# Optimization experiments

Measured on AMD Instinct MI355X. Metric: run time of the kernel, lower is better.

## Reference

```python
import jax, jax.numpy as jnp
import numpy as np

B, S, D, H = 2, 4096, 1024, 16
DH = D // H            # head dim = 64
W = 256                # one-sided attention window (attention_window // 2)
NC = S // W            # number of query chunks
NEG = -1e9


def setup_inputs() -> dict:
    key = jax.random.key(0)
    ks = jax.random.split(key, 8)
    sc = 0.02
    return {
        "hidden_states": jax.random.normal(ks[0], (B, S, D), jnp.float32),
        # additive float mask: 0 = local token, <0 = padding, >0 = global. All zeros here.
        "attention_mask": jnp.zeros((B, 1, 1, S), jnp.float32),
        "Wq": jax.random.normal(ks[1], (D, D), jnp.float32) * sc,
        "bq": jnp.zeros((D,), jnp.float32),
        "Wk": jax.random.normal(ks[2], (D, D), jnp.float32) * sc,
        "bk": jnp.zeros((D,), jnp.float32),
        "Wv": jax.random.normal(ks[3], (D, D), jnp.float32) * sc,
        "bv": jnp.zeros((D,), jnp.float32),
        "Wo": jax.random.normal(ks[4], (D, D), jnp.float32) * sc,
        "bo": jnp.zeros((D,), jnp.float32),
    }


def _heads(x, w, b):
    # [B,S,D] -> [B,H,S,DH]
    return (x @ w + b).reshape(B, S, H, DH).transpose(0, 2, 1, 3)


def _forward(hidden_states, attention_mask, Wq, bq, Wk, bk, Wv, bv, Wo, bo):
    mask = attention_mask[:, 0, 0, :]                    # [B,S] additive key mask
    q = _heads(hidden_states, Wq, bq) / jnp.sqrt(jnp.float32(DH))
    k = _heads(hidden_states, Wk, bk)
    v = _heads(hidden_states, Wv, bv)

    # Overlapping key/value chunks: chunk c covers padded positions [c*W, c*W+3W),
    # i.e. global keys [c*W - W, c*W + 2W) -- the union of the windows of its W queries.
    idx = jnp.arange(NC)[:, None] * W + jnp.arange(3 * W)[None, :]   # [NC,3W] into padded axis
    k_pad = jnp.pad(k, ((0, 0), (0, 0), (W, W), (0, 0)))
    v_pad = jnp.pad(v, ((0, 0), (0, 0), (W, W), (0, 0)))
    k_ch = k_pad[:, :, idx]                               # [B,H,NC,3W,DH]
    v_ch = v_pad[:, :, idx]                               # [B,H,NC,3W,DH]
    mask_ch = jnp.pad(mask, ((0, 0), (W, W)))[:, idx]     # [B,NC,3W]

    q_ch = q.reshape(B, H, NC, W, DH)
    scores = jnp.einsum('bhcqd,bhckd->bhcqk', q_ch, k_ch)  # [B,H,NC,W,3W]

    # Band mask: query local p attends key local o with 0 <= o - p <= 2W.
    rel = jnp.arange(3 * W)[None, :] - jnp.arange(W)[:, None]        # [W,3W]
    band = (rel >= 0) & (rel <= 2 * W)
    key_gidx = idx - W                                               # global key index
    valid = (key_gidx >= 0) & (key_gidx < S)                         # [NC,3W]
    allowed = band[None, :, :] & valid[:, None, :]                   # [NC,W,3W]

    scores = scores + mask_ch[:, None, :, None, :]
    scores = jnp.where(allowed[None, None], scores, NEG)
    probs = jax.nn.softmax(scores, axis=-1)

    out = jnp.einsum('bhcqk,bhckd->bhcqd', probs, v_ch)    # [B,H,NC,W,DH]
    out = out.reshape(B, H, S, DH).transpose(0, 2, 1, 3).reshape(B, S, D)
    return out @ Wo + bo


def reference(hidden_states, attention_mask, Wq, bq, Wk, bk, Wv, bv, Wo, bo):
    return _forward(hidden_states, attention_mask, Wq, bq, Wk, bk, Wv, bv, Wo, bo)
```

## Files before the change

### kernel.cpp

```cpp
#include <hip/hip_runtime.h>

typedef unsigned short u16;
typedef __bf16 bf16x8 __attribute__((ext_vector_type(8)));
typedef u16 u16x8 __attribute__((ext_vector_type(8)));
typedef float f32x4 __attribute__((ext_vector_type(4)));
typedef unsigned uint2v __attribute__((ext_vector_type(2)));

#define LOG2E 1.4426950408889634f

static __device__ __forceinline__ u16 f2bf(float f) {
    union { float f; unsigned u; } x; x.f = f;
    unsigned r = x.u + 0x7fffu + ((x.u >> 16) & 1u);
    return (u16)(r >> 16);
}

static __device__ __forceinline__ unsigned cvtpk(float lo, float hi) {
    unsigned r;
    asm("v_cvt_pk_bf16_f32 %0, %1, %2" : "=v"(r) : "v"(lo), "v"(hi));
    return r;
}

static __device__ __forceinline__ void gl_lds16(const void* g, void* l) {
    __builtin_amdgcn_global_load_lds(
        (const __attribute__((address_space(1))) void*)g,
        (__attribute__((address_space(3))) void*)l, 16, 0, 0);
}

__global__ __launch_bounds__(256) void cvt_k(const float* __restrict__ src,
                                             u16* __restrict__ dst, int n) {
    int i = (blockIdx.x * 256 + threadIdx.x) * 4;
    if (i < n) {
        float4 v = *(const float4*)(src + i);
        ushort4 o;
        o.x = f2bf(v.x); o.y = f2bf(v.y); o.z = f2bf(v.z); o.w = f2bf(v.w);
        *(ushort4*)(dst + i) = o;
    }
}

__global__ __launch_bounds__(256) void transw_k(const float* __restrict__ w0,
                                                const float* __restrict__ w1,
                                                const float* __restrict__ w2,
                                                const float* __restrict__ w3,
                                                u16* __restrict__ wt) {
    __shared__ float T[64][65];
    const float* src = (blockIdx.z == 0) ? w0 : (blockIdx.z == 1) ? w1
                     : (blockIdx.z == 2) ? w2 : w3;
    u16* dst = wt + (size_t)blockIdx.z * 1048576;
    const int k0 = blockIdx.x * 64, n0 = blockIdx.y * 64;
    const int rr = threadIdx.x >> 6, col = threadIdx.x & 63;
#pragma unroll
    for (int i = 0; i < 16; ++i) {
        int row = i * 4 + rr;
        T[row][col] = src[(size_t)(k0 + row) * 1024 + n0 + col];
    }
    __syncthreads();
#pragma unroll
    for (int i = 0; i < 16; ++i) {
        int row = i * 4 + rr;
        dst[(size_t)(n0 + row) * 1024 + k0 + col] = f2bf(T[col][row]);
    }
}

template<int MODE>
__global__ __launch_bounds__(256) void gemm_t(
    const u16* __restrict__ A, const u16* __restrict__ WT0,
    const float* __restrict__ b0, const float* __restrict__ b1,
    u16* __restrict__ o0, u16* __restrict__ o1, float* __restrict__ oF) {
    __shared__ alignas(16) u16 Al[128 * 64];
    __shared__ alignas(16) u16 Bl[128 * 64];

    const int tid = threadIdx.x;
    const int lane = tid & 63;
    const int wv = tid >> 6;
    const int wr = wv >> 1, wc = wv & 1;
    const int l15 = lane & 15, l4 = lane >> 4;

    const int mbase = blockIdx.x * 128;
    const int sel = (MODE == 0) ? (blockIdx.y >> 3) : 0;
    const int nb = (blockIdx.y & 7) * 128;

    const u16* Ab = A + (size_t)mbase * 1024;
    const u16* Bb = WT0 + (size_t)sel * 1048576 + (size_t)nb * 1024;

    const int lr8 = lane >> 3;
    const int ls = lane & 7;

    f32x4 acc[4][4] = {};

    auto stage = [&](const u16* src, u16* dstL, int k0) {
#pragma unroll
        for (int i = 0; i < 4; ++i) {
            int r = i * 32 + wv * 8 + lr8;
            gl_lds16(src + (size_t)r * 1024 + k0 + ((ls ^ (r & 7)) * 8),
                     dstL + (i * 2048 + wv * 512));
        }
    };

    for (int k0 = 0; k0 < 1024; k0 += 64) {
        stage(Ab, Al, k0);
        stage(Bb, Bl, k0);
        __syncthreads();

#pragma unroll
        for (int ks = 0; ks < 2; ++ks) {
            bf16x8 af[4], bfr[4];
#pragma unroll
            for (int mr = 0; mr < 4; ++mr) {
                int r = wr * 64 + mr * 16 + l15;
                af[mr] = *(const bf16x8*)(Al + r * 64 + (((ks * 4 + l4) ^ (r & 7)) * 8));
            }
#pragma unroll
            for (int nr = 0; nr < 4; ++nr) {
                int r = wc * 64 + nr * 16 + l15;
                bfr[nr] = *(const bf16x8*)(Bl + r * 64 + (((ks * 4 + l4) ^ (r & 7)) * 8));
            }
            if constexpr (MODE == 2) {
#pragma unroll
                for (int mr = 0; mr < 4; ++mr)
#pragma unroll
                    for (int nr = 0; nr < 4; ++nr)
                        acc[mr][nr] = __builtin_amdgcn_mfma_f32_16x16x32_bf16(
                            bfr[nr], af[mr], acc[mr][nr], 0, 0, 0);
            } else {
#pragma unroll
                for (int mr = 0; mr < 4; ++mr)
#pragma unroll
                    for (int nr = 0; nr < 4; ++nr)
                        acc[mr][nr] = __builtin_amdgcn_mfma_f32_16x16x32_bf16(
                            af[mr], bfr[nr], acc[mr][nr], 0, 0, 0);
            }
        }
        __syncthreads();
    }

    if constexpr (MODE == 2) {
#pragma unroll
        for (int mr = 0; mr < 4; ++mr) {
            int srow2 = mbase + wr * 64 + mr * 16 + l15;
            int b_ = srow2 >> 12, s_ = srow2 & 4095;
#pragma unroll
            for (int nr = 0; nr < 4; ++nr) {
                f32x4 bvv = *(const f32x4*)(b0 + nb + wc * 64 + nr * 16 + l4 * 4);
#pragma unroll
                for (int j = 0; j < 4; ++j) {
                    int c2 = nb + wc * 64 + nr * 16 + l4 * 4 + j;
                    float v = acc[mr][nr][j] + bvv[j];
                    o0[(((size_t)(b_ * 16 + (c2 >> 6)) * 64 + (c2 & 63)) * 4096) + s_] = f2bf(v);
                }
            }
        }
        return;
    }

    const float* bias = (MODE == 0 && sel == 1) ? b1 : b0;
    u16* oH = (sel == 0) ? o0 : o1;
    const float scale = (MODE == 0 && sel == 0) ? 0.125f * LOG2E : 1.0f;

#pragma unroll
    for (int mr = 0; mr < 4; ++mr)
#pragma unroll
        for (int nr = 0; nr < 4; ++nr) {
            int col = nb + wc * 64 + nr * 16 + l15;
            float bv_ = bias[col];
#pragma unroll
            for (int j = 0; j < 4; ++j) {
                int row = mbase + wr * 64 + mr * 16 + l4 * 4 + j;
                float v = (acc[mr][nr][j] + bv_) * scale;
                if constexpr (MODE == 0) {
                    int b_ = row >> 12, s_ = row & 4095;
                    int h_ = col >> 6, d_ = col & 63;
                    oH[(((size_t)(b_ * 16 + h_) * 4096) + s_) * 64 + d_] = f2bf(v);
                } else {
                    oF[(size_t)row * 1024 + col] = v;
                }
            }
        }
}

__global__ __launch_bounds__(256) void attn_k(
    const u16* __restrict__ Qh, const u16* __restrict__ Kh,
    const u16* __restrict__ Vt, const float* __restrict__ mask,
    u16* __restrict__ attnb) {
    __shared__ alignas(16) u16 Kt[2][4096];
    __shared__ alignas(16) u16 VtL[2][4096];
    __shared__ alignas(16) u16 Pl[4][2][1024];
    __shared__ alignas(16) float maskl[640];

    const int tid = threadIdx.x;
    const int lane = tid & 63;
    const int wv = tid >> 6;
    const int hw = blockIdx.x;
    const int lg = (hw & 7) * 128 + (hw >> 3);
    const int c = lg & 31;
    const int h = (lg >> 5) & 15;
    const int b = lg >> 9;

    const size_t bh = (size_t)(b * 16 + h) * 4096;
    const u16* Qb = Qh + bh * 64;
    const u16* Kb = Kh + bh * 64;
    const u16* Vb = Vt + bh * 64;
    const float* mb = mask + b * 4096;

    const int l15 = lane & 15;
    const int l4 = lane >> 4;
    const int qbase = c * 128 + wv * 32;
    const int gkbase = c * 128 - 256;

    bf16x8 qf[2][2];
#pragma unroll
    for (int qt = 0; qt < 2; ++qt)
#pragma unroll
        for (int kc = 0; kc < 2; ++kc)
            qf[qt][kc] = *(const bf16x8*)(Qb + (size_t)(qbase + qt * 16 + l15) * 64 + kc * 32 + l4 * 8);

    f32x4 Ov[4][2] = {};
    float lsum[2] = {0.f, 0.f};
    float m[2] = {-3.0e38f, -3.0e38f};

    auto stageK = [&](int buf, int gk) {
#pragma unroll
        for (int i = 0; i < 2; ++i) {
            int r = i * 32 + wv * 8 + (lane >> 3);
            int s = lane & 7;
            int key = min(max(gk + r, 0), 4095);
            gl_lds16(Kb + (size_t)key * 64 + ((s ^ (r & 7)) * 8),
                     &Kt[buf][(i * 32 + wv * 8) * 64]);
        }
    };
    auto stageV = [&](int buf, int gk) {
#pragma unroll
        for (int i = 0; i < 2; ++i) {
            int d = i * 32 + wv * 8 + (lane >> 3);
            int s = lane & 7;
            int col = min(max(gk + ((s ^ (d & 7)) * 8), 0), 4088);
            gl_lds16(Vb + (size_t)d * 4096 + col, &VtL[buf][(i * 32 + wv * 8) * 64]);
        }
    };

    stageK(0, gkbase);
    stageV(0, gkbase);
    for (int i = tid; i < 640; i += 256) {
        int gm = gkbase + i;
        maskl[i] = (gm >= 0 && gm < 4096) ? mb[gm] * LOG2E : 0.f;
    }
    __syncthreads();

    const int tmin = wv >> 1;
    const int tmaxw = 8 + (wv >> 1);

    for (int t = 0; t < 10; ++t) {
        const int cur = t & 1, nxt = cur ^ 1;
        const int gk0 = gkbase + t * 64;
        if (t < 9) { stageK(nxt, gk0 + 64); stageV(nxt, gk0 + 64); }

        if (t >= tmin && t <= tmaxw) {
            f32x4 mv[4];
#pragma unroll
            for (int kb = 0; kb < 4; ++kb)
                mv[kb] = *(const f32x4*)(maskl + t * 64 + kb * 16 + l4 * 4);

            f32x4 sc[4][2] = {};
            __builtin_amdgcn_s_setprio(1);
#pragma unroll
            for (int kc = 0; kc < 2; ++kc)
#pragma unroll
                for (int kb = 0; kb < 4; ++kb) {
                    int r = kb * 16 + l15;
                    bf16x8 kf = *(const bf16x8*)(&Kt[cur][r * 64 + (((kc * 4 + l4) ^ (r & 7)) * 8)]);
                    sc[kb][0] = __builtin_amdgcn_mfma_f32_16x16x32_bf16(kf, qf[0][kc], sc[kb][0], 0, 0, 0);
                    sc[kb][1] = __builtin_amdgcn_mfma_f32_16x16x32_bf16(kf, qf[1][kc], sc[kb][1], 0, 0, 0);
                }
            __builtin_amdgcn_s_setprio(0);

            const int dkq = gk0 - qbase;
            const bool full = (dkq >= -225) && (dkq <= 193) && (gk0 >= 0) && (gk0 <= 4032);
            if (full) {
#pragma unroll
                for (int kb = 0; kb < 4; ++kb)
#pragma unroll
                    for (int qt = 0; qt < 2; ++qt)
#pragma unroll
                        for (int j = 0; j < 4; ++j)
                            sc[kb][qt][j] += mv[kb][j];
            } else {
                const int kb0 = gk0 + l4 * 4;
                const int ub0 = kb0 - (qbase + l15) + 256;
#pragma unroll
                for (int kb = 0; kb < 4; ++kb)
#pragma unroll
                    for (int qt = 0; qt < 2; ++qt)
#pragma unroll
                        for (int j = 0; j < 4; ++j) {
                            float sv = sc[kb][qt][j] + mv[kb][j];
                            unsigned band = (unsigned)(ub0 + kb * 16 + j - qt * 16);
                            unsigned keyv = (unsigned)(kb0 + kb * 16 + j);
                            bool ok = (band <= 512u) && (keyv < 4096u);
                            sc[kb][qt][j] = ok ? sv : -3.0e9f;
                        }
            }

#pragma unroll
            for (int qt = 0; qt < 2; ++qt) {
                u16* Pw = &Pl[wv][qt][0];
                const int prow = l15 * 64;
                float mx = sc[0][qt][0];
#pragma unroll
                for (int kb = 0; kb < 4; ++kb)
#pragma unroll
                    for (int j = 0; j < 4; ++j) mx = fmaxf(mx, sc[kb][qt][j]);
                if (!__all(mx <= m[qt] + 8.0f)) {
                    mx = fmaxf(mx, __shfl_xor(mx, 16));
                    mx = fmaxf(mx, __shfl_xor(mx, 32));
                    float mnew = fmaxf(m[qt], mx);
                    float alpha = exp2f(m[qt] - mnew);
                    m[qt] = mnew;
                    lsum[qt] *= alpha;
#pragma unroll
                    for (int nd = 0; nd < 4; ++nd) Ov[nd][qt] *= alpha;
                }

                float s0 = 0.f;
#pragma unroll
                for (int kb = 0; kb < 4; ++kb) {
                    float p0 = exp2f(sc[kb][qt][0] - m[qt]);
                    float p1 = exp2f(sc[kb][qt][1] - m[qt]);
                    float p2 = exp2f(sc[kb][qt][2] - m[qt]);
                    float p3 = exp2f(sc[kb][qt][3] - m[qt]);
                    s0 += (p0 + p1) + (p2 + p3);
                    uint2v pk;
                    pk[0] = cvtpk(p0, p1);
                    pk[1] = cvtpk(p2, p3);
                    int g = (((kb * 2 + (l4 >> 1)) ^ (l15 & 7)) * 8) + (l4 & 1) * 4;
                    *(uint2v*)(Pw + prow + g) = pk;
                }
                lsum[qt] += s0;
            }

#pragma unroll
            for (int kc = 0; kc < 2; ++kc) {
                bf16x8 vf[4];
#pragma unroll
                for (int nd = 0; nd < 4; ++nd) {
                    int r2 = nd * 16 + l15;
                    vf[nd] = *(const bf16x8*)(&VtL[cur][r2 * 64 +
                        (((kc * 4 + l4) ^ (r2 & 7)) * 8)]);
                }
#pragma unroll
                for (int qt = 0; qt < 2; ++qt) {
                    bf16x8 pf = *(const bf16x8*)(&Pl[wv][qt][0] + l15 * 64 +
                                                 (((kc * 4 + l4) ^ (l15 & 7)) * 8));
                    __builtin_amdgcn_s_setprio(1);
#pragma unroll
                    for (int nd = 0; nd < 4; ++nd)
                        Ov[nd][qt] = __builtin_amdgcn_mfma_f32_16x16x32_bf16(vf[nd], pf, Ov[nd][qt], 0, 0, 0);
                    __builtin_amdgcn_s_setprio(0);
                }
            }
        }
        __syncthreads();
    }

    lsum[0] += __shfl_xor(lsum[0], 16);
    lsum[0] += __shfl_xor(lsum[0], 32);
    lsum[1] += __shfl_xor(lsum[1], 16);
    lsum[1] += __shfl_xor(lsum[1], 32);
    float inv0 = 1.0f / lsum[0];
    float inv1 = 1.0f / lsum[1];
#pragma unroll
    for (int qt = 0; qt < 2; ++qt) {
        float inv = qt ? inv1 : inv0;
        size_t rowb = ((size_t)b * 4096 + qbase + qt * 16 + l15) * 1024 + h * 64 + l4 * 4;
#pragma unroll
        for (int nd = 0; nd < 4; ++nd) {
            uint2v o;
            o[0] = cvtpk(Ov[nd][qt][0] * inv, Ov[nd][qt][1] * inv);
            o[1] = cvtpk(Ov[nd][qt][2] * inv, Ov[nd][qt][3] * inv);
            *(uint2v*)(&attnb[rowb + nd * 16]) = o;
        }
    }
}

extern "C" void kernel_launch(void* const* d_in, const int* in_sizes, int n_in,
                              void* d_out, int out_size, void* d_ws, size_t ws_size,
                              hipStream_t stream) {
    (void)in_sizes; (void)n_in; (void)out_size; (void)ws_size;
    const float* hid  = (const float*)d_in[0];
    const float* mask = (const float*)d_in[1];
    const float* Wq = (const float*)d_in[2];
    const float* bq = (const float*)d_in[3];
    const float* Wk = (const float*)d_in[4];
    const float* bk = (const float*)d_in[5];
    const float* Wv = (const float*)d_in[6];
    const float* bv = (const float*)d_in[7];
    const float* Wo = (const float*)d_in[8];
    const float* bo = (const float*)d_in[9];
    float* out = (float*)d_out;

    char* ws = (char*)d_ws;
    u16* hidb  = (u16*)(ws);
    u16* wt    = (u16*)(ws + (16u << 20));
    u16* Qh    = (u16*)(ws + (24u << 20));
    u16* Kh    = (u16*)(ws + (40u << 20));
    u16* Vtb   = (u16*)(ws + (56u << 20));
    u16* attnb = (u16*)(ws + (72u << 20));

    cvt_k<<<dim3(8192), dim3(256), 0, stream>>>(hid, hidb, 8388608);
    transw_k<<<dim3(16, 16, 4), dim3(256), 0, stream>>>(Wq, Wk, Wv, Wo, wt);
    gemm_t<0><<<dim3(64, 16), dim3(256), 0, stream>>>(hidb, wt, bq, bk,
                                                      Qh, Kh, (float*)nullptr);
    gemm_t<2><<<dim3(64, 8), dim3(256), 0, stream>>>(hidb, wt + 2 * 1048576, bv, (const float*)nullptr,
                                                     Vtb, (u16*)nullptr, (float*)nullptr);
    attn_k<<<dim3(1024), dim3(256), 0, stream>>>(Qh, Kh, Vtb, mask, attnb);
    gemm_t<1><<<dim3(64, 8), dim3(256), 0, stream>>>(attnb, wt + 3 * 1048576, bo, (const float*)nullptr,
                                                     (u16*)nullptr, (u16*)nullptr, out);
}
```

Before: 163.9 us.

## Fuse V projection into QK GEMM launch and skip zero-mask additions in attention

The separate V-projection GEMM launch is folded into the Q/K projection launch by extending the grid to 24 column blocks. Blocks with sel==2 run the swapped-operand MFMA loop and write the transposed V layout. This removes one kernel launch and its tail, and gives a larger grid. The attention kernel now checks whether any mask value in the block's window is nonzero and skips loading and adding the mask when all are zero, at the cost of one extra barrier and a shared flag.

```diff
diff --git a/kernel.cpp b/kernel.cpp
--- a/kernel.cpp
+++ b/kernel.cpp
@@ -7,6 +7,8 @@
 typedef unsigned uint2v __attribute__((ext_vector_type(2)));
 
 #define LOG2E 1.4426950408889634f
+
+template<bool B> struct BoolC { static constexpr bool value = B; };
 
 static __device__ __forceinline__ u16 f2bf(float f) {
     union { float f; unsigned u; } x; x.f = f;
@@ -65,7 +67,9 @@
 __global__ __launch_bounds__(256) void gemm_t(
     const u16* __restrict__ A, const u16* __restrict__ WT0,
     const float* __restrict__ b0, const float* __restrict__ b1,
-    u16* __restrict__ o0, u16* __restrict__ o1, float* __restrict__ oF) {
+    const float* __restrict__ b2,
+    u16* __restrict__ o0, u16* __restrict__ o1, u16* __restrict__ o2,
+    float* __restrict__ oF) {
     __shared__ alignas(16) u16 Al[128 * 64];
     __shared__ alignas(16) u16 Bl[128 * 64];
 
@@ -96,61 +100,66 @@
         }
     };
 
-    for (int k0 = 0; k0 < 1024; k0 += 64) {
-        stage(Ab, Al, k0);
-        stage(Bb, Bl, k0);
-        __syncthreads();
-
-#pragma unroll
-        for (int ks = 0; ks < 2; ++ks) {
-            bf16x8 af[4], bfr[4];
-#pragma unroll
-            for (int mr = 0; mr < 4; ++mr) {
-                int r = wr * 64 + mr * 16 + l15;
-                af[mr] = *(const bf16x8*)(Al + r * 64 + (((ks * 4 + l4) ^ (r & 7)) * 8));
-            }
-#pragma unroll
-            for (int nr = 0; nr < 4; ++nr) {
-                int r = wc * 64 + nr * 16 + l15;
-                bfr[nr] = *(const bf16x8*)(Bl + r * 64 + (((ks * 4 + l4) ^ (r & 7)) * 8));
-            }
-            if constexpr (MODE == 2) {
-#pragma unroll
-                for (int mr = 0; mr < 4; ++mr)
-#pragma unroll
-                    for (int nr = 0; nr < 4; ++nr)
-                        acc[mr][nr] = __builtin_amdgcn_mfma_f32_16x16x32_bf16(
-                            bfr[nr], af[mr], acc[mr][nr], 0, 0, 0);
-            } else {
-#pragma unroll
-                for (int mr = 0; mr < 4; ++mr)
-#pragma unroll
-                    for (int nr = 0; nr < 4; ++nr)
-                        acc[mr][nr] = __builtin_amdgcn_mfma_f32_16x16x32_bf16(
-                            af[mr], bfr[nr], acc[mr][nr], 0, 0, 0);
-            }
-        }
-        __syncthreads();
-    }
-
-    if constexpr (MODE == 2) {
+    auto kloop = [&](auto swap_c) {
+        constexpr bool SWAP = decltype(swap_c)::value;
+        for (int k0 = 0; k0 < 1024; k0 += 64) {
+            stage(Ab, Al, k0);
+            stage(Bb, Bl, k0);
+            __syncthreads();
+#pragma unroll
+            for (int ks = 0; ks < 2; ++ks) {
+                bf16x8 af[4], bfr[4];
+#pragma unroll
+                for (int mr = 0; mr < 4; ++mr) {
+                    int r = wr * 64 + mr * 16 + l15;
+                    af[mr] = *(const bf16x8*)(Al + r * 64 + (((ks * 4 + l4) ^ (r & 7)) * 8));
+                }
+#pragma unroll
+                for (int nr = 0; nr < 4; ++nr) {
+                    int r = wc * 64 + nr * 16 + l15;
+                    bfr[nr] = *(const bf16x8*)(Bl + r * 64 + (((ks * 4 + l4) ^ (r & 7)) * 8));
+                }
+                if constexpr (SWAP) {
+#pragma unroll
+                    for (int mr = 0; mr < 4; ++mr)
+#pragma unroll
+                        for (int nr = 0; nr < 4; ++nr)
+                            acc[mr][nr] = __builtin_amdgcn_mfma_f32_16x16x32_bf16(
+                                bfr[nr], af[mr], acc[mr][nr], 0, 0, 0);
+                } else {
+#pragma unroll
+                    for (int mr = 0; mr < 4; ++mr)
+#pragma unroll
+                        for (int nr = 0; nr < 4; ++nr)
+                            acc[mr][nr] = __builtin_amdgcn_mfma_f32_16x16x32_bf16(
+                                af[mr], bfr[nr], acc[mr][nr], 0, 0, 0);
+                }
+            }
+            __syncthreads();
+        }
+    };
+
+    if (MODE == 0 && sel == 2) {
+        kloop(BoolC<true>{});
 #pragma unroll
         for (int mr = 0; mr < 4; ++mr) {
             int srow2 = mbase + wr * 64 + mr * 16 + l15;
             int b_ = srow2 >> 12, s_ = srow2 & 4095;
 #pragma unroll
             for (int nr = 0; nr < 4; ++nr) {
-                f32x4 bvv = *(const f32x4*)(b0 + nb + wc * 64 + nr * 16 + l4 * 4);
+                f32x4 bvv = *(const f32x4*)(b2 + nb + wc * 64 + nr * 16 + l4 * 4);
 #pragma unroll
                 for (int j = 0; j < 4; ++j) {
                     int c2 = nb + wc * 64 + nr * 16 + l4 * 4 + j;
                     float v = acc[mr][nr][j] + bvv[j];
-                    o0[(((size_t)(b_ * 16 + (c2 >> 6)) * 64 + (c2 & 63)) * 4096) + s_] = f2bf(v);
+                    o2[(((size_t)(b_ * 16 + (c2 >> 6)) * 64 + (c2 & 63)) * 4096) + s_] = f2bf(v);
                 }
             }
         }
         return;
     }
+
+    kloop(BoolC<false>{});
 
     const float* bias = (MODE == 0 && sel == 1) ? b1 : b0;
     u16* oH = (sel == 0) ? o0 : o1;
@@ -185,6 +194,7 @@
     __shared__ alignas(16) u16 VtL[2][4096];
     __shared__ alignas(16) u16 Pl[4][2][1024];
     __shared__ alignas(16) float maskl[640];
+    __shared__ int anymask;
 
     const int tid = threadIdx.x;
     const int lane = tid & 63;
@@ -237,13 +247,23 @@
         }
     };
 
+    if (tid == 0) anymask = 0;
+    __syncthreads();
+
     stageK(0, gkbase);
     stageV(0, gkbase);
-    for (int i = tid; i < 640; i += 256) {
-        int gm = gkbase + i;
-        maskl[i] = (gm >= 0 && gm < 4096) ? mb[gm] * LOG2E : 0.f;
+    {
+        int f = 0;
+        for (int i = tid; i < 640; i += 256) {
+            int gm = gkbase + i;
+            float v = (gm >= 0 && gm < 4096) ? mb[gm] : 0.f;
+            f |= (v != 0.f);
+            maskl[i] = v * LOG2E;
+        }
+        if (f) anymask = 1;
     }
     __syncthreads();
+    const bool useMask = (anymask != 0);
 
     const int tmin = wv >> 1;
     const int tmaxw = 8 + (wv >> 1);
@@ -254,11 +274,6 @@
         if (t < 9) { stageK(nxt, gk0 + 64); stageV(nxt, gk0 + 64); }
 
         if (t >= tmin && t <= tmaxw) {
-            f32x4 mv[4];
-#pragma unroll
-            for (int kb = 0; kb < 4; ++kb)
-                mv[kb] = *(const f32x4*)(maskl + t * 64 + kb * 16 + l4 * 4);
-
             f32x4 sc[4][2] = {};
             __builtin_amdgcn_s_setprio(1);
 #pragma unroll
@@ -275,14 +290,29 @@
             const int dkq = gk0 - qbase;
             const bool full = (dkq >= -225) && (dkq <= 193) && (gk0 >= 0) && (gk0 <= 4032);
             if (full) {
-#pragma unroll
-                for (int kb = 0; kb < 4; ++kb)
-#pragma unroll
-                    for (int qt = 0; qt < 2; ++qt)
-#pragma unroll
-                        for (int j = 0; j < 4; ++j)
-                            sc[kb][qt][j] += mv[kb][j];
+                if (useMask) {
+                    f32x4 mv[4];
+#pragma unroll
+                    for (int kb = 0; kb < 4; ++kb)
+                        mv[kb] = *(const f32x4*)(maskl + t * 64 + kb * 16 + l4 * 4);
+#pragma unroll
+                    for (int kb = 0; kb < 4; ++kb)
+#pragma unroll
+                        for (int qt = 0; qt < 2; ++qt)
+#pragma unroll
+                            for (int j = 0; j < 4; ++j)
+                                sc[kb][qt][j] += mv[kb][j];
+                }
             } else {
+                f32x4 mv[4];
+                if (useMask) {
+#pragma unroll
+                    for (int kb = 0; kb < 4; ++kb)
+                        mv[kb] = *(const f32x4*)(maskl + t * 64 + kb * 16 + l4 * 4);
+                } else {
+#pragma unroll
+                    for (int kb = 0; kb < 4; ++kb) mv[kb] = f32x4{0.f, 0.f, 0.f, 0.f};
+                }
                 const int kb0 = gk0 + l4 * 4;
                 const int ub0 = kb0 - (qbase + l15) + 256;
 #pragma unroll
@@ -406,11 +436,10 @@
 
     cvt_k<<<dim3(8192), dim3(256), 0, stream>>>(hid, hidb, 8388608);
     transw_k<<<dim3(16, 16, 4), dim3(256), 0, stream>>>(Wq, Wk, Wv, Wo, wt);
-    gemm_t<0><<<dim3(64, 16), dim3(256), 0, stream>>>(hidb, wt, bq, bk,
-                                                      Qh, Kh, (float*)nullptr);
-    gemm_t<2><<<dim3(64, 8), dim3(256), 0, stream>>>(hidb, wt + 2 * 1048576, bv, (const float*)nullptr,
-                                                     Vtb, (u16*)nullptr, (float*)nullptr);
+    gemm_t<0><<<dim3(64, 24), dim3(256), 0, stream>>>(hidb, wt, bq, bk, bv,
+                                                      Qh, Kh, Vtb, (float*)nullptr);
     attn_k<<<dim3(1024), dim3(256), 0, stream>>>(Qh, Kh, Vtb, mask, attnb);
-    gemm_t<1><<<dim3(64, 8), dim3(256), 0, stream>>>(attnb, wt + 3 * 1048576, bo, (const float*)nullptr,
-                                                     (u16*)nullptr, (u16*)nullptr, out);
-}
+    gemm_t<1><<<dim3(64, 8), dim3(256), 0, stream>>>(attnb, wt + 3 * 1048576, bo, bo, bo,
+                                                     (u16*)nullptr, (u16*)nullptr, (u16*)nullptr,
+                                                     out);
+}
```

Measured after the change: 164.5 us. Within noise of the previous version (+0.4%).
